# Kernel optimization log

Measured on AMD Instinct MI355X. Metric: run time of the kernel, lower is better.

## Reference

```python
import jax, jax.numpy as jnp
import numpy as np
import math

N_EXP = 8
TOP_K = 2
CAPACITY_FACTOR = 1.25


def _capacity(num_tokens):
    cap = math.floor(TOP_K * CAPACITY_FACTOR * num_tokens / N_EXP)
    cap += cap % 2  # round up to even, as in nanoMoE
    return int(cap)


def setup_inputs() -> dict:
    key = jax.random.key(0)
    k1, k2, k3, k4 = jax.random.split(key, 4)
    B, C, d = 4, 1024, 1024
    x = jax.random.normal(k1, (B, C, d), dtype=jnp.float32)
    w_g = jax.random.normal(k2, (d, N_EXP), dtype=jnp.float32) * 0.02
    c_fc = jax.random.normal(k3, (N_EXP, d, 4 * d), dtype=jnp.float32) * 0.02
    c_proj = jax.random.normal(k4, (N_EXP, 4 * d, d), dtype=jnp.float32) * 0.02
    return {"x": x, "w_g": w_g, "c_fc": c_fc, "c_proj": c_proj}


def reference(x, w_g, c_fc, c_proj):
    B, C, d = x.shape
    T = B * C  # num_tokens (static)
    cap = _capacity(T)
    xt = x.reshape(T, d)

    # ---- Router (no noise: use_noisy_top_k=False, eval) ----
    logits = xt @ w_g                                   # [T, n_exp]
    top_v, top_i = jax.lax.top_k(logits, TOP_K)         # [T, k]
    full = jnp.full_like(logits, -jnp.inf)
    full = full.at[jnp.arange(T)[:, None], top_i].set(top_v)
    probs = jax.nn.softmax(full, axis=-1)               # [T, n_exp]

    # expert assignment mask and intra-expert rank (capacity dropping)
    exp_mask = jax.nn.one_hot(top_i, N_EXP, dtype=jnp.int32)       # [T, k, n_exp]
    exp_mask = jnp.transpose(exp_mask, (1, 0, 2))                  # [k, T, n_exp]
    exp_rank = jnp.cumsum(exp_mask.reshape(TOP_K * T, N_EXP), axis=0) - 1
    exp_rank = exp_rank.reshape(TOP_K, T, N_EXP)
    exp_mask = exp_mask * (exp_rank < cap).astype(jnp.int32)       # drop overflow
    exp_rank = jnp.sum(exp_mask * exp_rank, axis=-1)               # [k, T] slot id

    exp_weights = exp_mask.astype(x.dtype) * probs[None]           # [k, T, n_exp]
    rank_oh = jax.nn.one_hot(exp_rank, cap, dtype=x.dtype)         # [k, T, cap]
    # dense combine weights [T, n_exp, cap] (as in original code)
    cb_weight = jnp.einsum('kte,ktc->tec', exp_weights, rank_oh)
    sec_mask = (cb_weight != 0).astype(x.dtype)                    # dispatch mask

    # dispatch tokens into per-expert batches [n_exp, cap, d]
    exp_batches = jnp.einsum('tec,td->ecd', sec_mask, xt)

    # ---- MLPExperts: batched GEMM -> GELU (exact) -> batched GEMM ----
    h = jax.nn.gelu(jnp.einsum('ecd,edf->ecf', exp_batches, c_fc), approximate=False)
    exp_out = jnp.einsum('ecf,efd->ecd', h, c_proj)                # [n_exp, cap, d]

    # ---- weighted combine: [T, n_exp*cap] @ [n_exp*cap, d] ----
    out = cb_weight.reshape(T, N_EXP * cap) @ exp_out.reshape(N_EXP * cap, d)
    return out.reshape(B, C, d)
```

## Files before the change

kernel.cpp:

```cpp
#include <hip/hip_runtime.h>
#include <hip/hip_bf16.h>
#include <math.h>

#define T_TOK 4096
#define D     1024
#define DFF   4096
#define NEXP  8
#define CAP   1280
#define TOPK  2

typedef __bf16 bf16x8 __attribute__((ext_vector_type(8)));
typedef float floatx4 __attribute__((ext_vector_type(4)));

__device__ __forceinline__ unsigned short f2bf(float f) {
  union { float f; unsigned u; } un; un.f = f;
  unsigned r = un.u + 0x7FFF + ((un.u >> 16) & 1);
  return (unsigned short)(r >> 16);
}

__global__ __launch_bounds__(256) void router_kernel(
    const float* __restrict__ x, const float* __restrict__ wg,
    int* __restrict__ top_e, float* __restrict__ top_p) {
  int t = blockIdx.x * 4 + (threadIdx.x >> 6);
  int lane = threadIdx.x & 63;
  if (t >= T_TOK) return;
  const float* xr = x + (size_t)t * D;
  float acc[NEXP];
#pragma unroll
  for (int e = 0; e < NEXP; e++) acc[e] = 0.f;
  for (int dd = lane; dd < D; dd += 64) {
    float xv = xr[dd];
    const float* wr = wg + dd * NEXP;
#pragma unroll
    for (int e = 0; e < NEXP; e++) acc[e] += xv * wr[e];
  }
#pragma unroll
  for (int off = 32; off > 0; off >>= 1) {
#pragma unroll
    for (int e = 0; e < NEXP; e++) acc[e] += __shfl_xor(acc[e], off, 64);
  }
  if (lane == 0) {
    int b0 = 0; float v0 = acc[0];
    for (int e = 1; e < NEXP; e++) if (acc[e] > v0) { v0 = acc[e]; b0 = e; }
    int b1 = -1; float v1 = -INFINITY;
    for (int e = 0; e < NEXP; e++) if (e != b0 && acc[e] > v1) { v1 = acc[e]; b1 = e; }
    float e1 = expf(v1 - v0);
    float s = 1.0f + e1;
    top_e[t * 2 + 0] = b0; top_e[t * 2 + 1] = b1;
    top_p[t * 2 + 0] = 1.0f / s; top_p[t * 2 + 1] = e1 / s;
  }
}

__global__ __launch_bounds__(1024) void rank_kernel(
    const int* __restrict__ top_e, const float* __restrict__ top_p,
    int* __restrict__ slot_token, int* __restrict__ tok_slot,
    float* __restrict__ tok_w) {
  __shared__ int sc[1024][9];
  int tid = threadIdx.x;
  int base[NEXP];
#pragma unroll
  for (int e = 0; e < NEXP; e++) base[e] = 0;

  for (int k = 0; k < TOPK; k++) {
    int cnt[NEXP];
#pragma unroll
    for (int e = 0; e < NEXP; e++) cnt[e] = 0;
    int eloc[4];
#pragma unroll
    for (int i = 0; i < 4; i++) {
      int t = tid * 4 + i;
      int e = top_e[t * 2 + k];
      eloc[i] = e;
#pragma unroll
      for (int q = 0; q < NEXP; q++) cnt[q] += (q == e);
    }
    __syncthreads();
#pragma unroll
    for (int e = 0; e < NEXP; e++) sc[tid][e] = cnt[e];
    __syncthreads();
    for (int off = 1; off < 1024; off <<= 1) {
      int v[NEXP];
#pragma unroll
      for (int e = 0; e < NEXP; e++) v[e] = (tid >= off) ? sc[tid - off][e] : 0;
      __syncthreads();
#pragma unroll
      for (int e = 0; e < NEXP; e++) sc[tid][e] += v[e];
      __syncthreads();
    }
    int excl[NEXP];
#pragma unroll
    for (int e = 0; e < NEXP; e++) excl[e] = sc[tid][e] - cnt[e] + base[e];
    int nbase[NEXP];
#pragma unroll
    for (int e = 0; e < NEXP; e++) nbase[e] = base[e] + sc[1023][e];

    int run[NEXP];
#pragma unroll
    for (int e = 0; e < NEXP; e++) run[e] = 0;
#pragma unroll
    for (int i = 0; i < 4; i++) {
      int t = tid * 4 + i;
      int e = eloc[i];
      int r = 0;
#pragma unroll
      for (int q = 0; q < NEXP; q++)
        if (q == e) { r = excl[q] + run[q]; run[q]++; }
      if (r < CAP) {
        slot_token[e * CAP + r] = t;
        tok_slot[t * 2 + k] = e * CAP + r;
      } else {
        tok_slot[t * 2 + k] = -1;
      }
      tok_w[t * 2 + k] = top_p[t * 2 + k];
    }
#pragma unroll
    for (int e = 0; e < NEXP; e++) base[e] = nbase[e];
  }
}

__global__ __launch_bounds__(256) void gather_cvt_kernel(
    const float* __restrict__ x, const int* __restrict__ slot_token,
    unsigned short* __restrict__ xb) {
  int slot = blockIdx.x;
  int tok = slot_token[slot];
  int i = threadIdx.x;
  float4 v = make_float4(0.f, 0.f, 0.f, 0.f);
  if (tok >= 0) v = ((const float4*)(x + (size_t)tok * D))[i];
  ushort4 o;
  o.x = f2bf(v.x); o.y = f2bf(v.y); o.z = f2bf(v.z); o.w = f2bf(v.w);
  ((ushort4*)(xb + (size_t)slot * D))[i] = o;
}

__global__ __launch_bounds__(256) void transpose_cvt_kernel(
    const float* __restrict__ src, unsigned short* __restrict__ dst,
    int R, int Cc) {
  __shared__ float tile[32][33];
  int e = blockIdx.z;
  src += (size_t)e * R * Cc;
  dst += (size_t)e * R * Cc;
  int r0 = blockIdx.y * 32, c0 = blockIdx.x * 32;
  int tx = threadIdx.x & 31, ty = threadIdx.x >> 5;
#pragma unroll
  for (int i = 0; i < 32; i += 8)
    tile[ty + i][tx] = src[(size_t)(r0 + ty + i) * Cc + c0 + tx];
  __syncthreads();
#pragma unroll
  for (int i = 0; i < 32; i += 8)
    dst[(size_t)(c0 + ty + i) * R + r0 + tx] = f2bf(tile[tx][ty + i]);
}

template <bool GELU, bool OUT_BF16>
__global__ __launch_bounds__(256) void gemm_mfma_kernel(
    const unsigned short* __restrict__ A,
    const unsigned short* __restrict__ Bt,
    void* __restrict__ Cv, int M, int N, int K) {
  __shared__ unsigned short As[128 * 32];
  __shared__ unsigned short Bs[128 * 32];

  int e = blockIdx.z;
  A  += (size_t)e * M * K;
  Bt += (size_t)e * N * K;
  int row0 = blockIdx.y * 128, col0 = blockIdx.x * 128;

  int tid = threadIdx.x;
  int wave = tid >> 6, lane = tid & 63;

  int sr = lane >> 2;
  int sk = (lane & 3) * 8;
  size_t a_off0 = (size_t)(row0 + wave * 16 + sr) * K + sk;
  size_t a_off1 = a_off0 + (size_t)64 * K;
  size_t b_off0 = (size_t)(col0 + wave * 16 + sr) * K + sk;
  size_t b_off1 = b_off0 + (size_t)64 * K;
  unsigned short* as_dst0 = As + (wave * 16) * 32;
  unsigned short* as_dst1 = As + (wave * 16 + 64) * 32;
  unsigned short* bs_dst0 = Bs + (wave * 16) * 32;
  unsigned short* bs_dst1 = Bs + (wave * 16 + 64) * 32;

  int wm = (wave >> 1) * 64;
  int wn = (wave & 1) * 64;
  int fr = lane & 15;
  int fq = lane >> 4;

  floatx4 acc[4][4];
#pragma unroll
  for (int i = 0; i < 4; i++)
#pragma unroll
    for (int j = 0; j < 4; j++) acc[i][j] = (floatx4){0.f, 0.f, 0.f, 0.f};

  for (int k0 = 0; k0 < K; k0 += 32) {
    __builtin_amdgcn_global_load_lds(
        (const __attribute__((address_space(1))) unsigned int*)(A + a_off0 + k0),
        (__attribute__((address_space(3))) unsigned int*)as_dst0, 16, 0, 0);
    __builtin_amdgcn_global_load_lds(
        (const __attribute__((address_space(1))) unsigned int*)(A + a_off1 + k0),
        (__attribute__((address_space(3))) unsigned int*)as_dst1, 16, 0, 0);
    __builtin_amdgcn_global_load_lds(
        (const __attribute__((address_space(1))) unsigned int*)(Bt + b_off0 + k0),
        (__attribute__((address_space(3))) unsigned int*)bs_dst0, 16, 0, 0);
    __builtin_amdgcn_global_load_lds(
        (const __attribute__((address_space(1))) unsigned int*)(Bt + b_off1 + k0),
        (__attribute__((address_space(3))) unsigned int*)bs_dst1, 16, 0, 0);
    __syncthreads();

    bf16x8 af[4], bfr[4];
#pragma unroll
    for (int mi = 0; mi < 4; mi++)
      af[mi] = *(const bf16x8*)&As[(wm + mi * 16 + fr) * 32 + fq * 8];
#pragma unroll
    for (int ni = 0; ni < 4; ni++)
      bfr[ni] = *(const bf16x8*)&Bs[(wn + ni * 16 + fr) * 32 + fq * 8];
#pragma unroll
    for (int mi = 0; mi < 4; mi++)
#pragma unroll
      for (int ni = 0; ni < 4; ni++)
        acc[mi][ni] = __builtin_amdgcn_mfma_f32_16x16x32_bf16(
            af[mi], bfr[ni], acc[mi][ni], 0, 0, 0);
    __syncthreads();
  }

  int orow0 = row0 + wm + fq * 4;
  int ocol0 = col0 + wn + fr;
#pragma unroll
  for (int mi = 0; mi < 4; mi++) {
#pragma unroll
    for (int ni = 0; ni < 4; ni++) {
#pragma unroll
      for (int r = 0; r < 4; r++) {
        float v = acc[mi][ni][r];
        if (GELU) v = 0.5f * v * (1.f + erff(v * 0.70710678118654752f));
        size_t idx = (size_t)e * M * N + (size_t)(orow0 + mi * 16 + r) * N +
                     (ocol0 + ni * 16);
        if (OUT_BF16)
          ((unsigned short*)Cv)[idx] = f2bf(v);
        else
          ((float*)Cv)[idx] = v;
      }
    }
  }
}

__global__ __launch_bounds__(256) void combine_kernel(
    const float* __restrict__ eo, const int* __restrict__ tok_slot,
    const float* __restrict__ tok_w, float* __restrict__ out) {
  int t = blockIdx.x;
  int i = threadIdx.x;
  float4 acc = make_float4(0.f, 0.f, 0.f, 0.f);
#pragma unroll
  for (int k = 0; k < TOPK; k++) {
    int s = tok_slot[t * 2 + k];
    if (s >= 0) {
      float w = tok_w[t * 2 + k];
      float4 v = ((const float4*)(eo + (size_t)s * D))[i];
      acc.x += w * v.x; acc.y += w * v.y; acc.z += w * v.z; acc.w += w * v.w;
    }
  }
  ((float4*)(out + (size_t)t * D))[i] = acc;
}

extern "C" void kernel_launch(void* const* d_in, const int* in_sizes, int n_in,
                              void* d_out, int out_size, void* d_ws, size_t ws_size,
                              hipStream_t stream) {
  const float* x     = (const float*)d_in[0];
  const float* wg    = (const float*)d_in[1];
  const float* cfc   = (const float*)d_in[2];
  const float* cproj = (const float*)d_in[3];
  float* out = (float*)d_out;

  char* ws = (char*)d_ws;
  size_t off = 0;
  auto alloc = [&](size_t bytes) -> void* {
    void* p = ws + off;
    off += (bytes + 255) & ~(size_t)255;
    return p;
  };
  int*   top_e      = (int*)  alloc((size_t)T_TOK * 2 * 4);
  float* top_p      = (float*)alloc((size_t)T_TOK * 2 * 4);
  int*   slot_token = (int*)  alloc((size_t)NEXP * CAP * 4);
  int*   tok_slot   = (int*)  alloc((size_t)T_TOK * 2 * 4);
  float* tok_w      = (float*)alloc((size_t)T_TOK * 2 * 4);
  unsigned short* xb      = (unsigned short*)alloc((size_t)NEXP * CAP * D * 2);
  unsigned short* cfc_t   = (unsigned short*)alloc((size_t)NEXP * D * DFF * 2);
  unsigned short* cproj_t = (unsigned short*)alloc((size_t)NEXP * DFF * D * 2);
  unsigned short* h       = (unsigned short*)alloc((size_t)NEXP * CAP * DFF * 2);
  float* eo = (float*)xb;

  hipMemsetAsync(slot_token, 0xFF, (size_t)NEXP * CAP * 4, stream);

  transpose_cvt_kernel<<<dim3(DFF / 32, D / 32, NEXP), 256, 0, stream>>>(
      cfc, cfc_t, D, DFF);
  transpose_cvt_kernel<<<dim3(D / 32, DFF / 32, NEXP), 256, 0, stream>>>(
      cproj, cproj_t, DFF, D);

  router_kernel<<<T_TOK / 4, 256, 0, stream>>>(x, wg, top_e, top_p);
  rank_kernel<<<1, 1024, 0, stream>>>(top_e, top_p, slot_token, tok_slot, tok_w);
  gather_cvt_kernel<<<NEXP * CAP, 256, 0, stream>>>(x, slot_token, xb);

  gemm_mfma_kernel<true, true><<<dim3(DFF / 128, CAP / 128, NEXP), 256, 0, stream>>>(
      xb, cfc_t, h, CAP, DFF, D);
  gemm_mfma_kernel<false, false><<<dim3(D / 128, CAP / 128, NEXP), 256, 0, stream>>>(
      h, cproj_t, eo, CAP, D, DFF);

  combine_kernel<<<T_TOK, 256, 0, stream>>>(eo, tok_slot, tok_w, out);
}
```

Measured before the change: 670.8 us.

## Split-K second GEMM, widen GEMM blocks, vectorize transpose, shuffle-based rank scan

The rank kernel replaces its 1024-step shared-memory Hillis-Steele scan with wave-level shuffle scans plus a small cross-wave scan. It also clears slot_token itself, which removes the separate memset. The weight transpose-convert now uses 64x64 tiles with float4 loads and ushort4 stores. The expert GEMMs move to 512-thread blocks with 32-row wave tiles. The first GEMM's grid order is changed, and the second GEMM is split in two along K, writing two fp32 partial buffers that the combine kernel sums. In exchange, the down-projection writes and reads twice as much intermediate data, and the larger eo buffer now spills further into workspace that was previously used for the first GEMM's weights.

```diff
diff --git a/kernel.cpp b/kernel.cpp
--- a/kernel.cpp
+++ b/kernel.cpp
@@ -55,8 +55,14 @@
     const int* __restrict__ top_e, const float* __restrict__ top_p,
     int* __restrict__ slot_token, int* __restrict__ tok_slot,
     float* __restrict__ tok_w) {
-  __shared__ int sc[1024][9];
+  __shared__ int wsum[16][NEXP];
+  __shared__ int wscan[16][NEXP];
   int tid = threadIdx.x;
+  int lane = tid & 63, w = tid >> 6;
+
+  for (int s = tid; s < NEXP * CAP; s += 1024) slot_token[s] = -1;
+  __syncthreads();
+
   int base[NEXP];
 #pragma unroll
   for (int e = 0; e < NEXP; e++) base[e] = 0;
@@ -74,25 +80,39 @@
 #pragma unroll
       for (int q = 0; q < NEXP; q++) cnt[q] += (q == e);
     }
-    __syncthreads();
-#pragma unroll
-    for (int e = 0; e < NEXP; e++) sc[tid][e] = cnt[e];
-    __syncthreads();
-    for (int off = 1; off < 1024; off <<= 1) {
-      int v[NEXP];
-#pragma unroll
-      for (int e = 0; e < NEXP; e++) v[e] = (tid >= off) ? sc[tid - off][e] : 0;
-      __syncthreads();
-#pragma unroll
-      for (int e = 0; e < NEXP; e++) sc[tid][e] += v[e];
-      __syncthreads();
-    }
+    int inc[NEXP];
+#pragma unroll
+    for (int e = 0; e < NEXP; e++) inc[e] = cnt[e];
+    for (int off = 1; off < 64; off <<= 1) {
+#pragma unroll
+      for (int e = 0; e < NEXP; e++) {
+        int v = __shfl_up(inc[e], off, 64);
+        if (lane >= off) inc[e] += v;
+      }
+    }
+    if (lane == 63)
+#pragma unroll
+      for (int e = 0; e < NEXP; e++) wsum[w][e] = inc[e];
+    __syncthreads();
+    if (w == 0 && lane < 16) {
+      int s[NEXP];
+#pragma unroll
+      for (int e = 0; e < NEXP; e++) s[e] = wsum[lane][e];
+      for (int off = 1; off < 16; off <<= 1) {
+#pragma unroll
+        for (int e = 0; e < NEXP; e++) {
+          int v = __shfl_up(s[e], off, 64);
+          if (lane >= off) s[e] += v;
+        }
+      }
+#pragma unroll
+      for (int e = 0; e < NEXP; e++) wscan[lane][e] = s[e];
+    }
+    __syncthreads();
     int excl[NEXP];
 #pragma unroll
-    for (int e = 0; e < NEXP; e++) excl[e] = sc[tid][e] - cnt[e] + base[e];
-    int nbase[NEXP];
-#pragma unroll
-    for (int e = 0; e < NEXP; e++) nbase[e] = base[e] + sc[1023][e];
+    for (int e = 0; e < NEXP; e++)
+      excl[e] = inc[e] - cnt[e] + (w ? wscan[w - 1][e] : 0) + base[e];
 
     int run[NEXP];
 #pragma unroll
@@ -114,7 +134,8 @@
       tok_w[t * 2 + k] = top_p[t * 2 + k];
     }
 #pragma unroll
-    for (int e = 0; e < NEXP; e++) base[e] = nbase[e];
+    for (int e = 0; e < NEXP; e++) base[e] += wscan[15][e];
+    __syncthreads();
   }
 }
 
@@ -134,83 +155,94 @@
 __global__ __launch_bounds__(256) void transpose_cvt_kernel(
     const float* __restrict__ src, unsigned short* __restrict__ dst,
     int R, int Cc) {
-  __shared__ float tile[32][33];
+  __shared__ float tile[64][65];
   int e = blockIdx.z;
   src += (size_t)e * R * Cc;
   dst += (size_t)e * R * Cc;
-  int r0 = blockIdx.y * 32, c0 = blockIdx.x * 32;
-  int tx = threadIdx.x & 31, ty = threadIdx.x >> 5;
-#pragma unroll
-  for (int i = 0; i < 32; i += 8)
-    tile[ty + i][tx] = src[(size_t)(r0 + ty + i) * Cc + c0 + tx];
+  int r0 = blockIdx.y * 64, c0 = blockIdx.x * 64;
+  int tr = threadIdx.x >> 4;
+  int tc = (threadIdx.x & 15) * 4;
+#pragma unroll
+  for (int i = 0; i < 64; i += 16) {
+    float4 v = *(const float4*)(src + (size_t)(r0 + tr + i) * Cc + c0 + tc);
+    tile[tr + i][tc + 0] = v.x;
+    tile[tr + i][tc + 1] = v.y;
+    tile[tr + i][tc + 2] = v.z;
+    tile[tr + i][tc + 3] = v.w;
+  }
   __syncthreads();
 #pragma unroll
-  for (int i = 0; i < 32; i += 8)
-    dst[(size_t)(c0 + ty + i) * R + r0 + tx] = f2bf(tile[tx][ty + i]);
-}
-
-template <bool GELU, bool OUT_BF16>
-__global__ __launch_bounds__(256) void gemm_mfma_kernel(
+  for (int i = 0; i < 64; i += 16) {
+    int c = tr + i, r = tc;
+    ushort4 o;
+    o.x = f2bf(tile[r + 0][c]);
+    o.y = f2bf(tile[r + 1][c]);
+    o.z = f2bf(tile[r + 2][c]);
+    o.w = f2bf(tile[r + 3][c]);
+    *(ushort4*)(dst + (size_t)(c0 + c) * R + r0 + r) = o;
+  }
+}
+
+template <int MODE>
+__global__ __launch_bounds__(512) void gemm_mfma_kernel(
     const unsigned short* __restrict__ A,
     const unsigned short* __restrict__ Bt,
-    void* __restrict__ Cv, int M, int N, int K) {
+    void* __restrict__ Cv) {
+  constexpr int MM = CAP;
+  constexpr int NN = (MODE == 0) ? DFF : D;
+  constexpr int LDA = (MODE == 0) ? D : DFF;
+  constexpr int KLEN = (MODE == 0) ? D : DFF / 2;
+
   __shared__ unsigned short As[128 * 32];
   __shared__ unsigned short Bs[128 * 32];
 
-  int e = blockIdx.z;
-  A  += (size_t)e * M * K;
-  Bt += (size_t)e * N * K;
-  int row0 = blockIdx.y * 128, col0 = blockIdx.x * 128;
-
+  int e, yt, xt, kh;
+  if (MODE == 0) {
+    e = blockIdx.x; yt = blockIdx.y; xt = blockIdx.z; kh = 0;
+  } else {
+    xt = blockIdx.x; yt = blockIdx.y; e = blockIdx.z >> 1; kh = blockIdx.z & 1;
+  }
+
+  const unsigned short* Ae = A + (size_t)e * MM * LDA + (size_t)kh * KLEN;
+  const unsigned short* Be = Bt + (size_t)e * NN * LDA + (size_t)kh * KLEN;
+
+  int row0 = yt * 128, col0 = xt * 128;
   int tid = threadIdx.x;
   int wave = tid >> 6, lane = tid & 63;
 
-  int sr = lane >> 2;
-  int sk = (lane & 3) * 8;
-  size_t a_off0 = (size_t)(row0 + wave * 16 + sr) * K + sk;
-  size_t a_off1 = a_off0 + (size_t)64 * K;
-  size_t b_off0 = (size_t)(col0 + wave * 16 + sr) * K + sk;
-  size_t b_off1 = b_off0 + (size_t)64 * K;
-  unsigned short* as_dst0 = As + (wave * 16) * 32;
-  unsigned short* as_dst1 = As + (wave * 16 + 64) * 32;
-  unsigned short* bs_dst0 = Bs + (wave * 16) * 32;
-  unsigned short* bs_dst1 = Bs + (wave * 16 + 64) * 32;
-
-  int wm = (wave >> 1) * 64;
+  size_t a_off = (size_t)(row0 + (tid >> 2)) * LDA + (tid & 3) * 8;
+  size_t b_off = (size_t)(col0 + (tid >> 2)) * LDA + (tid & 3) * 8;
+  unsigned short* as_dst = As + tid * 8;
+  unsigned short* bs_dst = Bs + tid * 8;
+
+  int wm = (wave >> 1) * 32;
   int wn = (wave & 1) * 64;
-  int fr = lane & 15;
-  int fq = lane >> 4;
-
-  floatx4 acc[4][4];
-#pragma unroll
-  for (int i = 0; i < 4; i++)
+  int fr = lane & 15, fq = lane >> 4;
+
+  floatx4 acc[2][4];
+#pragma unroll
+  for (int i = 0; i < 2; i++)
 #pragma unroll
     for (int j = 0; j < 4; j++) acc[i][j] = (floatx4){0.f, 0.f, 0.f, 0.f};
 
-  for (int k0 = 0; k0 < K; k0 += 32) {
+  for (int k0 = 0; k0 < KLEN; k0 += 32) {
     __builtin_amdgcn_global_load_lds(
-        (const __attribute__((address_space(1))) unsigned int*)(A + a_off0 + k0),
-        (__attribute__((address_space(3))) unsigned int*)as_dst0, 16, 0, 0);
+        (const __attribute__((address_space(1))) unsigned int*)(Ae + a_off + k0),
+        (__attribute__((address_space(3))) unsigned int*)as_dst, 16, 0, 0);
     __builtin_amdgcn_global_load_lds(
-        (const __attribute__((address_space(1))) unsigned int*)(A + a_off1 + k0),
-        (__attribute__((address_space(3))) unsigned int*)as_dst1, 16, 0, 0);
-    __builtin_amdgcn_global_load_lds(
-        (const __attribute__((address_space(1))) unsigned int*)(Bt + b_off0 + k0),
-        (__attribute__((address_space(3))) unsigned int*)bs_dst0, 16, 0, 0);
-    __builtin_amdgcn_global_load_lds(
-        (const __attribute__((address_space(1))) unsigned int*)(Bt + b_off1 + k0),
-        (__attribute__((address_space(3))) unsigned int*)bs_dst1, 16, 0, 0);
-    __syncthreads();
-
-    bf16x8 af[4], bfr[4];
-#pragma unroll
-    for (int mi = 0; mi < 4; mi++)
+        (const __attribute__((address_space(1))) unsigned int*)(Be + b_off + k0),
+        (__attribute__((address_space(3))) unsigned int*)bs_dst, 16, 0, 0);
+    __syncthreads();
+
+    bf16x8 af[2], bfr[4];
+#pragma unroll
+    for (int mi = 0; mi < 2; mi++)
       af[mi] = *(const bf16x8*)&As[(wm + mi * 16 + fr) * 32 + fq * 8];
 #pragma unroll
     for (int ni = 0; ni < 4; ni++)
       bfr[ni] = *(const bf16x8*)&Bs[(wn + ni * 16 + fr) * 32 + fq * 8];
 #pragma unroll
-    for (int mi = 0; mi < 4; mi++)
+    for (int mi = 0; mi < 2; mi++)
 #pragma unroll
       for (int ni = 0; ni < 4; ni++)
         acc[mi][ni] = __builtin_amdgcn_mfma_f32_16x16x32_bf16(
@@ -220,22 +252,28 @@
 
   int orow0 = row0 + wm + fq * 4;
   int ocol0 = col0 + wn + fr;
-#pragma unroll
-  for (int mi = 0; mi < 4; mi++) {
-#pragma unroll
-    for (int ni = 0; ni < 4; ni++) {
-#pragma unroll
-      for (int r = 0; r < 4; r++) {
-        float v = acc[mi][ni][r];
-        if (GELU) v = 0.5f * v * (1.f + erff(v * 0.70710678118654752f));
-        size_t idx = (size_t)e * M * N + (size_t)(orow0 + mi * 16 + r) * N +
-                     (ocol0 + ni * 16);
-        if (OUT_BF16)
-          ((unsigned short*)Cv)[idx] = f2bf(v);
-        else
-          ((float*)Cv)[idx] = v;
-      }
-    }
+  if (MODE == 0) {
+    unsigned short* Cb = (unsigned short*)Cv + (size_t)e * MM * NN;
+#pragma unroll
+    for (int mi = 0; mi < 2; mi++)
+#pragma unroll
+      for (int ni = 0; ni < 4; ni++)
+#pragma unroll
+        for (int r = 0; r < 4; r++) {
+          float v = acc[mi][ni][r];
+          v = 0.5f * v * (1.f + erff(v * 0.70710678118654752f));
+          Cb[(size_t)(orow0 + mi * 16 + r) * NN + (ocol0 + ni * 16)] = f2bf(v);
+        }
+  } else {
+    float* Cf = (float*)Cv + ((size_t)kh * NEXP + e) * MM * NN;
+#pragma unroll
+    for (int mi = 0; mi < 2; mi++)
+#pragma unroll
+      for (int ni = 0; ni < 4; ni++)
+#pragma unroll
+        for (int r = 0; r < 4; r++)
+          Cf[(size_t)(orow0 + mi * 16 + r) * NN + (ocol0 + ni * 16)] =
+              acc[mi][ni][r];
   }
 }
 
@@ -244,14 +282,19 @@
     const float* __restrict__ tok_w, float* __restrict__ out) {
   int t = blockIdx.x;
   int i = threadIdx.x;
+  const size_t half = (size_t)NEXP * CAP * D;
   float4 acc = make_float4(0.f, 0.f, 0.f, 0.f);
 #pragma unroll
   for (int k = 0; k < TOPK; k++) {
     int s = tok_slot[t * 2 + k];
     if (s >= 0) {
       float w = tok_w[t * 2 + k];
-      float4 v = ((const float4*)(eo + (size_t)s * D))[i];
-      acc.x += w * v.x; acc.y += w * v.y; acc.z += w * v.z; acc.w += w * v.w;
+      float4 v0 = ((const float4*)(eo + (size_t)s * D))[i];
+      float4 v1 = ((const float4*)(eo + half + (size_t)s * D))[i];
+      acc.x += w * (v0.x + v1.x);
+      acc.y += w * (v0.y + v1.y);
+      acc.z += w * (v0.z + v1.z);
+      acc.w += w * (v0.w + v1.w);
     }
   }
   ((float4*)(out + (size_t)t * D))[i] = acc;
@@ -284,21 +327,19 @@
   unsigned short* h       = (unsigned short*)alloc((size_t)NEXP * CAP * DFF * 2);
   float* eo = (float*)xb;
 
-  hipMemsetAsync(slot_token, 0xFF, (size_t)NEXP * CAP * 4, stream);
-
-  transpose_cvt_kernel<<<dim3(DFF / 32, D / 32, NEXP), 256, 0, stream>>>(
+  transpose_cvt_kernel<<<dim3(DFF / 64, D / 64, NEXP), 256, 0, stream>>>(
       cfc, cfc_t, D, DFF);
-  transpose_cvt_kernel<<<dim3(D / 32, DFF / 32, NEXP), 256, 0, stream>>>(
+  transpose_cvt_kernel<<<dim3(D / 64, DFF / 64, NEXP), 256, 0, stream>>>(
       cproj, cproj_t, DFF, D);
 
   router_kernel<<<T_TOK / 4, 256, 0, stream>>>(x, wg, top_e, top_p);
   rank_kernel<<<1, 1024, 0, stream>>>(top_e, top_p, slot_token, tok_slot, tok_w);
   gather_cvt_kernel<<<NEXP * CAP, 256, 0, stream>>>(x, slot_token, xb);
 
-  gemm_mfma_kernel<true, true><<<dim3(DFF / 128, CAP / 128, NEXP), 256, 0, stream>>>(
-      xb, cfc_t, h, CAP, DFF, D);
-  gemm_mfma_kernel<false, false><<<dim3(D / 128, CAP / 128, NEXP), 256, 0, stream>>>(
-      h, cproj_t, eo, CAP, D, DFF);
+  gemm_mfma_kernel<0><<<dim3(NEXP, CAP / 128, DFF / 128), 512, 0, stream>>>(
+      xb, cfc_t, h);
+  gemm_mfma_kernel<1><<<dim3(D / 128, CAP / 128, NEXP * 2), 512, 0, stream>>>(
+      h, cproj_t, eo);
 
   combine_kernel<<<T_TOK, 256, 0, stream>>>(eo, tok_slot, tok_w, out);
 }
```

Result: faster. 634.0 us (-5.5%).
